# Kernel optimization log

Measured on AMD Instinct MI355X. Metric: run time of the kernel, lower is better.

The kernel has to match this reference:

```python
import jax, jax.numpy as jnp
import numpy as np

NEG_INF = -1000000000.0

N, T, D, H = 2, 4096, 512, 8
S = D // H  # size_per_head = 64


def setup_inputs() -> dict:
    key = jax.random.key(0)
    ks = jax.random.split(key, 6)
    scale = 1.0 / np.sqrt(D)
    return {
        "query": jax.random.normal(ks[0], (N, T, D), dtype=jnp.float32),
        "reference": jax.random.normal(ks[1], (N, T, D), dtype=jnp.float32),
        "padding_mask": jnp.zeros((N, 1, 1, T), dtype=jnp.float32),
        "Wq": jax.random.normal(ks[2], (D, H, S), dtype=jnp.float32) * scale,
        "Wk": jax.random.normal(ks[3], (D, H, S), dtype=jnp.float32) * scale,
        "Wv": jax.random.normal(ks[4], (D, H, S), dtype=jnp.float32) * scale,
        "Wo": jax.random.normal(ks[5], (H, S, D), dtype=jnp.float32) * scale,
    }


def reference(query, reference, padding_mask, Wq, Wk, Wv, Wo):
    # split projections: [N,T,D] x [D,H,S] -> [N,T,H,S]
    q = jnp.einsum("NTD,DHS->NTHS", query, Wq) * (S ** -0.5)
    k = jnp.einsum("NTD,DHS->NTHS", reference, Wk)
    v = jnp.einsum("NTD,DHS->NTHS", reference, Wv)
    # scores [N,H,Q,R]; mask is 0/1, scaled by NEG_INF (as in source)
    scores = jnp.einsum("NQHS,NRHS->NHQR", q, k) + padding_mask * NEG_INF
    probs = jax.nn.softmax(scores, axis=3)
    # dropout is identity (training=False)
    ctx = jnp.einsum("NHQR,NRHS->NQHS", probs, v)
    # merge projection: [N,Q,H,S] x [H,S,D] -> [N,Q,D]
    return jnp.einsum("NTHS,HSD->NTD", ctx, Wo)
```

## Files before the change

### kernel.cpp

```cpp
#include <hip/hip_runtime.h>
#include <stdint.h>

using u16    = unsigned short;
using u32    = unsigned int;
using short8 = __attribute__((ext_vector_type(8))) short;
using s16x4  = __attribute__((ext_vector_type(4))) short;
using f32x4  = __attribute__((ext_vector_type(4))) float;
using f32x16 = __attribute__((ext_vector_type(16))) float;
using i32x4  = __attribute__((ext_vector_type(4))) int;

constexpr float LOG2E = 1.44269504088896340736f;


__device__ __forceinline__ u16 f2bf(float f) {
  uint32_t u = __builtin_bit_cast(uint32_t, f);
  return (u16)((u + 0x7fffu + ((u >> 16) & 1u)) >> 16);
}

__device__ __forceinline__ void gload16(const void* g, void* l) {
  __builtin_amdgcn_global_load_lds(
      (const __attribute__((address_space(1))) unsigned int*)g,
      (__attribute__((address_space(3))) unsigned int*)l, 16, 0, 0);
}

__device__ __forceinline__ u32 cvtpk_bf16(float lo, float hi) {
  u32 r;
  asm("v_cvt_pk_bf16_f32 %0, %1, %2" : "=v"(r) : "v"(lo), "v"(hi));
  return r;
}

__device__ __forceinline__ f32x16 zero16() {
  f32x16 z;
#pragma unroll
  for (int i = 0; i < 16; ++i) z[i] = 0.f;
  return z;
}

__device__ __forceinline__ short8 ldfrag(const u16* s, int row, int kbyte) {
  int phys = (row << 7) + (kbyte ^ ((row & 7) << 4));
  return *(const short8*)((const char*)s + phys);
}

__global__ __launch_bounds__(256) void prep_kernel(
    const float4* __restrict__ qin, const float4* __restrict__ rin,
    const float* __restrict__ mask,
    const float* __restrict__ wq, const float* __restrict__ wk,
    const float* __restrict__ wv, const float* __restrict__ wo,
    u16* __restrict__ xq, u16* __restrict__ xr,
    u16* __restrict__ wqt, u16* __restrict__ wkt,
    u16* __restrict__ wvt, u16* __restrict__ wot,
    u16* __restrict__ kfr) {
  const int gid = blockIdx.x * blockDim.x + threadIdx.x;
  const int stride = gridDim.x * blockDim.x;
  for (int i = gid; i < (2 * 4096 * 512) / 4; i += stride) {
    float4 a = qin[i], b = rin[i];
    s16x4 va = {(short)f2bf(a.x), (short)f2bf(a.y), (short)f2bf(a.z), (short)f2bf(a.w)};
    s16x4 vb = {(short)f2bf(b.x), (short)f2bf(b.y), (short)f2bf(b.z), (short)f2bf(b.w)};
    *(s16x4*)(xq + i * 4) = va;
    *(s16x4*)(xr + i * 4) = vb;
  }
  for (int i = gid; i < 512 * 512; i += stride) {
    int orow = i >> 9, ocol = i & 511;
    int si = ocol * 512 + orow;
    wqt[i] = f2bf(wq[si]);
    wkt[i] = f2bf(wk[si]);
    wvt[i] = f2bf(wv[si]);
    wot[i] = f2bf(wo[si]);
  }
  for (int i = gid; i < 16 * 4096; i += stride) {
    int head = i >> 12, key = i & 4095;
    int nn = head >> 3;
    float mt = mask[nn * 4096 + key] * (-1.0e9f * LOG2E);
    int tile = key >> 5, lqk = key & 31;
    u16* base = kfr + (((size_t)(head * 128 + tile)) * 5 + 4) * 512;
    u16* p0 = base + (size_t)lqk * 8;
    u16* p1 = base + (size_t)(32 + lqk) * 8;
    p0[0] = f2bf(mt);
#pragma unroll
    for (int j = 1; j < 8; ++j) p0[j] = 0;
#pragma unroll
    for (int j = 0; j < 8; ++j) p1[j] = 0;
  }
}

__device__ __forceinline__ void gemm_core(const u16* __restrict__ A, const u16* __restrict__ Bt,
                                          int K, u16* As, u16* Bs, int tm0, int tn0,
                                          f32x4 acc[4][4]) {
  const int tid = threadIdx.x;
  const int wv = tid >> 6, ln = tid & 63;
  const int lr = ln & 15, hi = ln >> 4;
  const int wr = wv >> 1, wc = wv & 1;
  const size_t rowbytes = (size_t)K * 2;
  for (int k0 = 0; k0 < K; k0 += 64) {
    __syncthreads();
    const char* Ab = (const char*)A + (size_t)tm0 * rowbytes + (size_t)k0 * 2;
    const char* Bb = (const char*)Bt + (size_t)tn0 * rowbytes + (size_t)k0 * 2;
#pragma unroll
    for (int c = 0; c < 4; ++c) {
      int lin = wv * 4096 + c * 1024 + ln * 16;
      int row = lin >> 7;
      int cb = (lin & 127) ^ ((row & 7) << 4);
      gload16(Ab + (size_t)row * rowbytes + cb, (char*)As + wv * 4096 + c * 1024);
      gload16(Bb + (size_t)row * rowbytes + cb, (char*)Bs + wv * 4096 + c * 1024);
    }
    __syncthreads();
#pragma unroll
    for (int ks = 0; ks < 2; ++ks) {
      short8 af[4], bf[4];
#pragma unroll
      for (int m = 0; m < 4; ++m) af[m] = ldfrag(As, wr * 64 + m * 16 + lr, ks * 64 + hi * 16);
#pragma unroll
      for (int n = 0; n < 4; ++n) bf[n] = ldfrag(Bs, wc * 64 + n * 16 + lr, ks * 64 + hi * 16);
#pragma unroll
      for (int m = 0; m < 4; ++m)
#pragma unroll
        for (int n = 0; n < 4; ++n)
          acc[m][n] = __builtin_amdgcn_mfma_f32_16x16x32_bf16(af[m], bf[n], acc[m][n], 0, 0, 0);
    }
  }
}

__global__ __launch_bounds__(256) void qkv_gemm(
    const u16* __restrict__ xq, const u16* __restrict__ xr,
    const u16* __restrict__ wqt, const u16* __restrict__ wkt, const u16* __restrict__ wvt,
    u16* __restrict__ qo, u16* __restrict__ kfr, u16* __restrict__ vfr) {
  __shared__ u16 As[128 * 64];
  __shared__ u16 Bs[128 * 64];
  const int z = blockIdx.z;
  const u16* A  = (z == 0) ? xq : xr;
  const u16* Bt = (z == 0) ? wqt : (z == 1) ? wkt : wvt;
  const int tm0 = blockIdx.x * 128, tn0 = blockIdx.y * 128;
  f32x4 acc[4][4];
#pragma unroll
  for (int m = 0; m < 4; ++m)
#pragma unroll
    for (int n = 0; n < 4; ++n) { f32x4 zz = {0.f, 0.f, 0.f, 0.f}; acc[m][n] = zz; }
  gemm_core(A, Bt, 512, As, Bs, tm0, tn0, acc);

  const int tid = threadIdx.x, wv = tid >> 6, ln = tid & 63, lr = ln & 15, hi = ln >> 4;
  const int wr = wv >> 1, wc = wv & 1;
  const float scale = (z == 0) ? 0.125f * LOG2E : 1.0f;
#pragma unroll
  for (int m = 0; m < 4; ++m) {
#pragma unroll
    for (int n = 0; n < 4; ++n) {
#pragma unroll
      for (int r = 0; r < 4; ++r) {
        int rg = tm0 + wr * 64 + m * 16 + hi * 4 + r;
        int cg = tn0 + wc * 64 + n * 16 + lr;
        int nb = rg >> 12, t = rg & 4095;
        int h = cg >> 6, s = cg & 63;
        int head = nb * 8 + h;
        u16 b = f2bf(acc[m][n][r] * scale);
        if (z == 0) {
          qo[((size_t)head * 4096 + t) * 64 + s] = b;
        } else if (z == 1) {
          int tile = t >> 5, lqk = t & 31;
          int ks = s >> 4, hh = (s >> 3) & 1, j = s & 7;
          kfr[((((size_t)(head * 128 + tile)) * 5 + ks) * 64 + hh * 32 + lqk) * 8 + j] = b;
        } else {
          int tile = t >> 5, w5 = t & 31;
          int ks = w5 >> 4, hh = (w5 >> 3) & 1, j = w5 & 7;
          int st = s >> 5, lqs = s & 31;
          vfr[((((size_t)(head * 128 + tile)) * 4 + ks * 2 + st) * 64 + hh * 32 + lqs) * 8 + j] = b;
        }
      }
    }
  }
}

__global__ __launch_bounds__(512, 2) void attn8_kernel(
    const u16* __restrict__ q, const char* __restrict__ kfr, const char* __restrict__ vfr,
    u16* __restrict__ ctx) {
  __shared__ float cmb[4][32][64];
  __shared__ float cl[4][64];
  const int id = blockIdx.x;
  const int xcd = id & 7, slot = id >> 3;
  const int head = xcd * 2 + (slot >> 4);
  const int qb = slot & 15;
  const int n = head >> 3, h = head & 7;
  const int tid = threadIdx.x, wv = tid >> 6, ln = tid & 63;
  const int lq = ln & 31, hi = ln >> 5, hi4 = hi * 4;
  const int qt = wv & 3, kg = wv >> 2;
  const int q0 = qb * 256 + qt * 64;

  short8 qfa[5], qfb[5];
  {
    const char* qp = (const char*)(q + (size_t)head * 4096 * 64) + (size_t)(q0 + lq) * 128 + hi * 16;
#pragma unroll
    for (int ks = 0; ks < 4; ++ks) {
      qfa[ks] = *(const short8*)(qp + ks * 32);
      qfb[ks] = *(const short8*)(qp + 32 * 128 + ks * 32);
    }
    short8 z = {0, 0, 0, 0, 0, 0, 0, 0};
    if (hi == 0) z[0] = (short)0x3F80;
    qfa[4] = z;
    qfb[4] = z;
  }

  const char* kp = kfr + (size_t)head * 655360 + (size_t)(kg * 64) * 5120 + ln * 16;
  const char* vp = vfr + (size_t)head * 524288 + (size_t)(kg * 64) * 4096 + ln * 16;

  short8 kA[5];
#pragma unroll
  for (int s = 0; s < 5; ++s) kA[s] = *(const short8*)(kp + s * 1024);
  kp += 5120;

  f32x16 cacc0a = zero16(), cacc1a = zero16();
  f32x16 cacc0b = zero16(), cacc1b = zero16();
  float lra = 0.f, lrb = 0.f;

  auto process = [&](f32x16& S0, float& lrun, f32x16& c0, f32x16& c1,
                     short8 vA[4]) {
    float p0[16];
#pragma unroll
    for (int r = 0; r < 16; ++r) p0[r] = __builtin_amdgcn_exp2f(S0[r]);
    {
      float a[16];
#pragma unroll
      for (int r = 0; r < 16; ++r) a[r] = p0[r];
#pragma unroll
      for (int d = 8; d > 0; d >>= 1)
#pragma unroll
        for (int r = 0; r < d; ++r) a[r] += a[r + d];
      lrun += a[0] + __shfl_xor(a[0], 32);
    }
    short8 pa0, pa1;
#define SHF32(x) ((u32)__shfl_xor((int)(x), 32))
    {
      u32 A01 = cvtpk_bf16(p0[0], p0[1]), B23 = cvtpk_bf16(p0[2], p0[3]);
      u32 C45 = cvtpk_bf16(p0[4], p0[5]), D67 = cvtpk_bf16(p0[6], p0[7]);
      u32 E89 = cvtpk_bf16(p0[8], p0[9]), F01 = cvtpk_bf16(p0[10], p0[11]);
      u32 G23 = cvtpk_bf16(p0[12], p0[13]), H45 = cvtpk_bf16(p0[14], p0[15]);
      u32 A01x = SHF32(A01), B23x = SHF32(B23), C45x = SHF32(C45), D67x = SHF32(D67);
      u32 E89x = SHF32(E89), F01x = SHF32(F01), G23x = SHF32(G23), H45x = SHF32(H45);
      i32x4 fa = {(int)(hi ? C45x : A01), (int)(hi ? D67x : B23),
                  (int)(hi ? C45 : A01x), (int)(hi ? D67 : B23x)};
      i32x4 fb = {(int)(hi ? G23x : E89), (int)(hi ? H45x : F01),
                  (int)(hi ? G23 : E89x), (int)(hi ? H45 : F01x)};
      pa0 = __builtin_bit_cast(short8, fa);
      pa1 = __builtin_bit_cast(short8, fb);
    }
#undef SHF32
    __builtin_amdgcn_s_setprio(1);
    c0 = __builtin_amdgcn_mfma_f32_32x32x16_bf16(pa0, vA[0], c0, 0, 0, 0);
    c1 = __builtin_amdgcn_mfma_f32_32x32x16_bf16(pa0, vA[1], c1, 0, 0, 0);
    c0 = __builtin_amdgcn_mfma_f32_32x32x16_bf16(pa1, vA[2], c0, 0, 0, 0);
    c1 = __builtin_amdgcn_mfma_f32_32x32x16_bf16(pa1, vA[3], c1, 0, 0, 0);
    __builtin_amdgcn_s_setprio(0);
  };

  for (int it = 0; it < 64; ++it) {
    short8 vA[4];
#pragma unroll
    for (int s = 0; s < 4; ++s) vA[s] = *(const short8*)(vp + s * 1024);
    vp += 4096;

    f32x16 Sa = zero16(), Sb = zero16();
    __builtin_amdgcn_s_setprio(1);
#pragma unroll
    for (int ks = 0; ks < 5; ++ks) Sa = __builtin_amdgcn_mfma_f32_32x32x16_bf16(kA[ks], qfa[ks], Sa, 0, 0, 0);
#pragma unroll
    for (int ks = 0; ks < 5; ++ks) Sb = __builtin_amdgcn_mfma_f32_32x32x16_bf16(kA[ks], qfb[ks], Sb, 0, 0, 0);
    __builtin_amdgcn_s_setprio(0);

    short8 kN[5];
#pragma unroll
    for (int s = 0; s < 5; ++s) kN[s] = *(const short8*)(kp + s * 1024);
    kp += 5120;

    process(Sa, lra, cacc0a, cacc1a, vA);
    process(Sb, lrb, cacc0b, cacc1b, vA);

#pragma unroll
    for (int s = 0; s < 5; ++s) kA[s] = kN[s];
  }

  u16* cp = ctx + (size_t)(n * 4096 + q0) * 512 + h * 64;
  if (kg == 1) {
#pragma unroll
    for (int r = 0; r < 16; ++r) {
      cmb[qt][r][ln] = cacc0a[r];
      cmb[qt][r + 16][ln] = cacc1a[r];
    }
    cl[qt][ln] = lra;
  }
  __syncthreads();
  if (kg == 0) {
#pragma unroll
    for (int r = 0; r < 16; ++r) {
      cacc0a[r] += cmb[qt][r][ln];
      cacc1a[r] += cmb[qt][r + 16][ln];
    }
    lra += cl[qt][ln];
    float li = 1.0f / lra;
    int lii = __builtin_bit_cast(int, li);
#pragma unroll
    for (int r = 0; r < 16; ++r) {
      int cr = (r & 3) + ((r >> 2) << 3) + hi4;
      float inv = __builtin_bit_cast(float, __builtin_amdgcn_ds_bpermute(cr << 2, lii));
      cp[(size_t)cr * 512 + lq] = f2bf(cacc0a[r] * inv);
      cp[(size_t)cr * 512 + 32 + lq] = f2bf(cacc1a[r] * inv);
    }
  }
  __syncthreads();
  if (kg == 1) {
#pragma unroll
    for (int r = 0; r < 16; ++r) {
      cmb[qt][r][ln] = cacc0b[r];
      cmb[qt][r + 16][ln] = cacc1b[r];
    }
    cl[qt][ln] = lrb;
  }
  __syncthreads();
  if (kg == 0) {
#pragma unroll
    for (int r = 0; r < 16; ++r) {
      cacc0b[r] += cmb[qt][r][ln];
      cacc1b[r] += cmb[qt][r + 16][ln];
    }
    lrb += cl[qt][ln];
    float li = 1.0f / lrb;
    int lii = __builtin_bit_cast(int, li);
    u16* cpb = cp + (size_t)32 * 512;
#pragma unroll
    for (int r = 0; r < 16; ++r) {
      int cr = (r & 3) + ((r >> 2) << 3) + hi4;
      float inv = __builtin_bit_cast(float, __builtin_amdgcn_ds_bpermute(cr << 2, lii));
      cpb[(size_t)cr * 512 + lq] = f2bf(cacc0b[r] * inv);
      cpb[(size_t)cr * 512 + 32 + lq] = f2bf(cacc1b[r] * inv);
    }
  }
}

__global__ __launch_bounds__(256) void out_gemm(
    const u16* __restrict__ ctx, const u16* __restrict__ wot, float* __restrict__ out) {
  __shared__ u16 As[128 * 64];
  __shared__ u16 Bs[128 * 64];
  const int tm0 = blockIdx.x * 128, tn0 = blockIdx.y * 128;
  f32x4 acc[4][4];
#pragma unroll
  for (int m = 0; m < 4; ++m)
#pragma unroll
    for (int n = 0; n < 4; ++n) { f32x4 zz = {0.f, 0.f, 0.f, 0.f}; acc[m][n] = zz; }
  gemm_core(ctx, wot, 512, As, Bs, tm0, tn0, acc);

  const int tid = threadIdx.x, wv = tid >> 6, ln = tid & 63, lr = ln & 15, hi = ln >> 4;
  const int wr = wv >> 1, wc = wv & 1;
#pragma unroll
  for (int m = 0; m < 4; ++m)
#pragma unroll
    for (int n = 0; n < 4; ++n)
#pragma unroll
      for (int r = 0; r < 4; ++r) {
        int rg = tm0 + wr * 64 + m * 16 + hi * 4 + r;
        int cg = tn0 + wc * 64 + n * 16 + lr;
        out[(size_t)rg * 512 + cg] = acc[m][n][r];
      }
}

extern "C" void kernel_launch(void* const* d_in, const int* in_sizes, int n_in,
                              void* d_out, int out_size, void* d_ws, size_t ws_size,
                              hipStream_t stream) {
  (void)in_sizes; (void)n_in; (void)out_size; (void)ws_size;
  const float* qin  = (const float*)d_in[0];
  const float* rin  = (const float*)d_in[1];
  const float* mask = (const float*)d_in[2];
  const float* wq   = (const float*)d_in[3];
  const float* wk   = (const float*)d_in[4];
  const float* wv   = (const float*)d_in[5];
  const float* wo   = (const float*)d_in[6];

  char* ws = (char*)d_ws;
  u16* xq   = (u16*)(ws + 0);
  u16* ctx  = (u16*)(ws + 0);
  u16* xr   = (u16*)(ws + 8388608);
  u16* wqt  = (u16*)(ws + 16777216);
  u16* wkt  = (u16*)(ws + 17301504);
  u16* wvt  = (u16*)(ws + 17825792);
  u16* wot  = (u16*)(ws + 18350080);
  u16* qo   = (u16*)(ws + 18874368);
  u16* kfr  = (u16*)(ws + 27262976);
  u16* vfr  = (u16*)(ws + 37748736);

  prep_kernel<<<2048, 256, 0, stream>>>((const float4*)qin, (const float4*)rin, mask,
                                        wq, wk, wv, wo, xq, xr, wqt, wkt, wvt, wot, kfr);
  qkv_gemm<<<dim3(64, 4, 3), 256, 0, stream>>>(xq, xr, wqt, wkt, wvt, qo, kfr, vfr);
  attn8_kernel<<<256, 512, 0, stream>>>(qo, (const char*)kfr, (const char*)vfr, ctx);
  out_gemm<<<dim3(64, 4), 256, 0, stream>>>(ctx, wot, (float*)d_out);
}
```

Measured before the change: 139.3 us.

## Double-buffer K/V tiles in LDS via async global-to-LDS loads

The attention kernel used to load K and V fragments straight from global memory into registers, with a one-step register prefetch for K only. It now stages each iteration's K and V tiles for both key groups into a double-buffered shared-memory area using global_load_lds, prefetching the next tile while computing the current one, then reads fragments from LDS. This hides global latency and shares each block's loads among its waves. In exchange it adds a block-wide barrier every iteration and raises LDS use to 36KB per block, which may limit occupancy.

Result: slower. 146.8 us (+5.4%).

```diff
diff --git a/kernel.cpp b/kernel.cpp
--- a/kernel.cpp
+++ b/kernel.cpp
@@ -169,15 +169,14 @@
   }
 }
 
-__global__ __launch_bounds__(512, 2) void attn8_kernel(
+__global__ __launch_bounds__(512, 2) void attn10_kernel(
     const u16* __restrict__ q, const char* __restrict__ kfr, const char* __restrict__ vfr,
     u16* __restrict__ ctx) {
-  __shared__ float cmb[4][32][64];
-  __shared__ float cl[4][64];
+  __shared__ __align__(16) char smem[36864];
   const int id = blockIdx.x;
-  const int xcd = id & 7, slot = id >> 3;
-  const int head = xcd * 2 + (slot >> 4);
-  const int qb = slot & 15;
+  const int xcd = id & 7, slot7 = id >> 3;
+  const int head = xcd * 2 + (slot7 >> 4);
+  const int qb = slot7 & 15;
   const int n = head >> 3, h = head & 7;
   const int tid = threadIdx.x, wv = tid >> 6, ln = tid & 63;
   const int lq = ln & 31, hi = ln >> 5, hi4 = hi * 4;
@@ -198,13 +197,25 @@
     qfb[4] = z;
   }
 
-  const char* kp = kfr + (size_t)head * 655360 + (size_t)(kg * 64) * 5120 + ln * 16;
-  const char* vp = vfr + (size_t)head * 524288 + (size_t)(kg * 64) * 4096 + ln * 16;
-
-  short8 kA[5];
-#pragma unroll
-  for (int s = 0; s < 5; ++s) kA[s] = *(const short8*)(kp + s * 1024);
-  kp += 5120;
+  const char* kh = kfr + (size_t)head * 655360;
+  const char* vh = vfr + (size_t)head * 524288;
+
+  auto stage = [&](int b, int it) {
+    char* base = smem + b * 18432;
+#pragma unroll
+    for (int s = wv; s < 18; s += 8) {
+      const char* src;
+      if (s < 10) {
+        int strm = (s >= 5) ? 1 : 0, ks = s - strm * 5;
+        src = kh + (size_t)(strm * 64 + it) * 5120 + ks * 1024 + ln * 16;
+      } else {
+        int j = s - 10;
+        int strm = (j >= 4) ? 1 : 0, sv = j - strm * 4;
+        src = vh + (size_t)(strm * 64 + it) * 4096 + sv * 1024 + ln * 16;
+      }
+      gload16(src, base + (s << 10));
+    }
+  };
 
   f32x16 cacc0a = zero16(), cacc1a = zero16();
   f32x16 cacc0b = zero16(), cacc1b = zero16();
@@ -250,11 +261,21 @@
     __builtin_amdgcn_s_setprio(0);
   };
 
+  stage(0, 0);
+  __syncthreads();
+
   for (int it = 0; it < 64; ++it) {
-    short8 vA[4];
-#pragma unroll
-    for (int s = 0; s < 4; ++s) vA[s] = *(const short8*)(vp + s * 1024);
-    vp += 4096;
+    const int cur = it & 1;
+    if (it < 63) stage(cur ^ 1, it + 1);
+    const char* base = smem + cur * 18432;
+    const char* kbase = base + (kg * 5) * 1024;
+    const char* vbase = base + (10 + kg * 4) * 1024;
+
+    short8 kA[5], vA[4];
+#pragma unroll
+    for (int s = 0; s < 5; ++s) kA[s] = *(const short8*)(kbase + (s << 10) + (ln << 4));
+#pragma unroll
+    for (int s = 0; s < 4; ++s) vA[s] = *(const short8*)(vbase + (s << 10) + (ln << 4));
 
     f32x16 Sa = zero16(), Sb = zero16();
     __builtin_amdgcn_s_setprio(1);
@@ -264,18 +285,14 @@
     for (int ks = 0; ks < 5; ++ks) Sb = __builtin_amdgcn_mfma_f32_32x32x16_bf16(kA[ks], qfb[ks], Sb, 0, 0, 0);
     __builtin_amdgcn_s_setprio(0);
 
-    short8 kN[5];
-#pragma unroll
-    for (int s = 0; s < 5; ++s) kN[s] = *(const short8*)(kp + s * 1024);
-    kp += 5120;
-
     process(Sa, lra, cacc0a, cacc1a, vA);
     process(Sb, lrb, cacc0b, cacc1b, vA);
 
-#pragma unroll
-    for (int s = 0; s < 5; ++s) kA[s] = kN[s];
-  }
-
+    __syncthreads();
+  }
+
+  float (*cmb)[32][64] = reinterpret_cast<float(*)[32][64]>(smem);
+  float (*cl)[64]      = reinterpret_cast<float(*)[64]>(smem + 32768);
   u16* cp = ctx + (size_t)(n * 4096 + q0) * 512 + h * 64;
   if (kg == 1) {
 #pragma unroll
@@ -386,6 +403,6 @@
   prep_kernel<<<2048, 256, 0, stream>>>((const float4*)qin, (const float4*)rin, mask,
                                         wq, wk, wv, wo, xq, xr, wqt, wkt, wvt, wot, kfr);
   qkv_gemm<<<dim3(64, 4, 3), 256, 0, stream>>>(xq, xr, wqt, wkt, wvt, qo, kfr, vfr);
-  attn8_kernel<<<256, 512, 0, stream>>>(qo, (const char*)kfr, (const char*)vfr, ctx);
+  attn10_kernel<<<256, 512, 0, stream>>>(qo, (const char*)kfr, (const char*)vfr, ctx);
   out_gemm<<<dim3(64, 4), 256, 0, stream>>>(ctx, wot, (float*)d_out);
 }
```
